# Kernel tuning notes

Measured on AMD Instinct MI355X. Metric: run time of the kernel, lower is better.

Reference implementation:

```python
import jax, jax.numpy as jnp
import numpy as np
import math

EPS_NORM = 1e-12
BN_EPS = 1e-5


def _l2norm(x):
    n = jnp.sqrt(jnp.sum(x * x, axis=-1, keepdims=True))
    return x / jnp.maximum(n, EPS_NORM)


def setup_inputs() -> dict:
    key = jax.random.key(0)
    ks = jax.random.split(key, 16)
    b, c, t, l = 16, 32, 16, 256
    s = 0.05
    return {
        "x": jax.random.normal(ks[0], (b, c, t, l), jnp.float32),
        "q_w": jax.random.normal(ks[1], (c, c), jnp.float32) * s,
        "q_b": jax.random.normal(ks[2], (c,), jnp.float32) * s,
        "k_w": jax.random.normal(ks[3], (c, c), jnp.float32) * s,
        "k_b": jax.random.normal(ks[4], (c,), jnp.float32) * s,
        "v_w": jax.random.normal(ks[5], (c, c), jnp.float32) * s,
        "v_b": jax.random.normal(ks[6], (c,), jnp.float32) * s,
        "m_w": jax.random.normal(ks[7], (c, c), jnp.float32) * s,
        "m_b": jax.random.normal(ks[8], (c,), jnp.float32) * s,
        "pre_prompt": jax.random.normal(ks[9], (1, c, 1, l), jnp.float32) * s,
        "conv_w": jax.random.normal(ks[10], (c, c, 9, 1), jnp.float32) * s,
        "conv_b": jax.random.normal(ks[11], (c,), jnp.float32) * s,
        "bn_gamma": jnp.ones((c,), jnp.float32),
        "bn_beta": jnp.zeros((c,), jnp.float32),
        "lin_w": jax.random.normal(ks[12], (l, l), jnp.float32) * s,
        "lin_b": jax.random.normal(ks[13], (l,), jnp.float32) * s,
        "atten_flag": 1,
    }


def reference(x, q_w, q_b, k_w, k_b, v_w, v_b, m_w, m_b, pre_prompt,
              conv_w, conv_b, bn_gamma, bn_beta, lin_w, lin_b, atten_flag):
    b, c, t, l = x.shape
    nh = 8
    hd = c // nh

    xp = jnp.transpose(x, (0, 2, 3, 1))  # (b,t,l,c)

    def heads(w, bias):
        h = xp @ w.T + bias
        h = h.reshape(b, t, l, nh, hd).transpose(0, 1, 3, 2, 4)  # (b,t,nh,l,hd)
        return _l2norm(h)

    q = heads(q_w, q_b)
    k = heads(k_w, k_b)
    v = heads(v_w, v_b)

    atten = jnp.einsum('bthld,bthmd->bthlm', q, k) / math.sqrt(hd)
    atten = jax.nn.softmax(atten, axis=-1)
    o = jnp.einsum('bthlm,bthmd->bthld', atten, v)  # (b,t,nh,l,hd)
    o = o.transpose(0, 1, 3, 2, 4).reshape(b, t, l, c)
    o = o @ m_w.T + m_b
    xo = jnp.transpose(o, (0, 3, 1, 2))  # (b,c,t,l)

    pre = jnp.broadcast_to(pre_prompt, (b, c, 1, l))
    con = jnp.concatenate([xo[:, :, :8], pre], axis=2)  # (b,c,9,l)

    # ConvNormAct: Conv2d (VALID, kernel (9,1)) + BatchNorm2d (batch stats) + ReLU
    h = jax.lax.conv_general_dilated(
        con, conv_w, window_strides=(1, 1), padding='VALID',
        dimension_numbers=('NCHW', 'OIHW', 'NCHW'))  # (b,c,1,l)
    h = h + conv_b[None, :, None, None]
    mean = jnp.mean(h, axis=(0, 2, 3), keepdims=True)
    var = jnp.var(h, axis=(0, 2, 3), keepdims=True)
    h = (h - mean) * jax.lax.rsqrt(var + BN_EPS)
    h = h * bn_gamma[None, :, None, None] + bn_beta[None, :, None, None]
    h = jax.nn.relu(h)

    p = h @ lin_w.T + lin_b  # Linear over token_len axis
    p = xo[:, :, 2:3] - p
    return jnp.concatenate([xo[:, :, :8], p], axis=2)  # (b,c,9,l)
```

## Files before the change

### kernel.cpp

```cpp
#include <hip/hip_runtime.h>
#include <hip/hip_bf16.h>


typedef __fp16 h2 __attribute__((ext_vector_type(2)));

#define O_OFF  0u
#define XO_OFF 2097152u
#define H_OFF  6291456u
#define S_OFF  6815744u

__device__ __forceinline__ int probe_f32(const unsigned short* graw) {
    return graw[0] == 0;
}
template<typename T> __device__ __forceinline__ float ldv(const T* p, long i);
template<> __device__ __forceinline__ float ldv<float>(const float* p, long i) {
    return p[i];
}
template<> __device__ __forceinline__ float ldv<__hip_bfloat16>(const __hip_bfloat16* p, long i) {
    return __bfloat162float(p[i]);
}
template<typename T> __device__ __forceinline__ void stv(T* p, size_t i, float v);
template<> __device__ __forceinline__ void stv<float>(float* p, size_t i, float v) {
    p[i] = v;
}
template<> __device__ __forceinline__ void stv<__hip_bfloat16>(__hip_bfloat16* p, size_t i, float v) {
    p[i] = __float2bfloat16(v);
}
__device__ __forceinline__ h2 pkh2(float a, float b) {
    return __builtin_amdgcn_cvt_pkrtz(a, b);
}
__device__ __forceinline__ float bflo(unsigned int u) {
    union { unsigned int i; float f; } c; c.i = u << 16; return c.f;
}
__device__ __forceinline__ float bfhi(unsigned int u) {
    union { unsigned int i; float f; } c; c.i = u & 0xffff0000u; return c.f;
}
#if __has_builtin(__builtin_amdgcn_fdot2)
__device__ __forceinline__ float fdot2(h2 a, h2 b, float c) {
    return __builtin_amdgcn_fdot2(a, b, c, false);
}
#else
__device__ __forceinline__ float fdot2(h2 a, h2 b, float c) {
    return fmaf((float)a[0], (float)b[0], fmaf((float)a[1], (float)b[1], c));
}
#endif
union KVrow { uint4 u; h2 h[4]; };

template<typename T>
__device__ __forceinline__ void attn_phase(
    const T* __restrict__ x,
    const T* __restrict__ qw, const T* __restrict__ qb,
    const T* __restrict__ kw, const T* __restrict__ kb,
    const T* __restrict__ vw, const T* __restrict__ vb,
    unsigned short* __restrict__ O, char* smem)
{
    uint4* KV = (uint4*)smem;
    float (*WL)[4][32] = (float (*)[4][32])(smem + 4096);
    float (*BL)[4]     = (float (*)[4])(smem + 5632);

    const int tid = threadIdx.x;
    const int blk = blockIdx.x;
    const int h = blk & 7, bt = blk >> 3;
    const int b = bt >> 3, t = bt & 7;
    const int h4 = h * 4;

    for (int e = tid; e < 384; e += 128) {
        int p = e >> 7, r = e & 127;
        const T* W = (p == 0) ? qw : ((p == 1) ? kw : vw);
        WL[p][r >> 5][r & 31] = ldv(W, (long)(h4 + (r >> 5)) * 32 + (r & 31));
    }
    if (tid < 12) {
        int p = tid >> 2, j = tid & 3;
        const T* B = (p == 0) ? qb : ((p == 1) ? kb : vb);
        BL[p][j] = ldv(B, h4 + j);
    }

    float xv0[32], xv1[32];
    #pragma unroll
    for (int c = 0; c < 32; c++) {
        const long xb = (((long)b * 32 + c) * 16 + t) * 256 + tid;
        xv0[c] = ldv(x, xb);
        xv1[c] = ldv(x, xb + 128);
    }
    __syncthreads();

    float4 pr0[3], pr1[3];
    #pragma unroll
    for (int p = 0; p < 3; p++) {
        float a0[4], a1[4];
        #pragma unroll
        for (int j = 0; j < 4; j++) { a0[j] = BL[p][j]; a1[j] = a0[j]; }
        #pragma unroll
        for (int c0 = 0; c0 < 32; c0 += 4) {
            float4 w0 = *(const float4*)&WL[p][0][c0];
            float4 w1 = *(const float4*)&WL[p][1][c0];
            float4 w2 = *(const float4*)&WL[p][2][c0];
            float4 w3 = *(const float4*)&WL[p][3][c0];
            const float* wj[4] = {(const float*)&w0, (const float*)&w1,
                                  (const float*)&w2, (const float*)&w3};
            #pragma unroll
            for (int cc = 0; cc < 4; cc++) {
                float x0 = xv0[c0+cc], x1 = xv1[c0+cc];
                #pragma unroll
                for (int j = 0; j < 4; j++) {
                    a0[j] = fmaf(x0, wj[j][cc], a0[j]);
                    a1[j] = fmaf(x1, wj[j][cc], a1[j]);
                }
            }
        }
        float s20 = a0[0]*a0[0] + a0[1]*a0[1] + a0[2]*a0[2] + a0[3]*a0[3];
        float s21 = a1[0]*a1[0] + a1[1]*a1[1] + a1[2]*a1[2] + a1[3]*a1[3];
        float i0 = 1.0f / fmaxf(sqrtf(s20), 1e-12f);
        float i1 = 1.0f / fmaxf(sqrtf(s21), 1e-12f);
        if (p == 0) { i0 *= 0.7213475204444817f; i1 *= 0.7213475204444817f; }
        pr0[p] = make_float4(a0[0]*i0, a0[1]*i0, a0[2]*i0, a0[3]*i0);
        pr1[p] = make_float4(a1[0]*i1, a1[1]*i1, a1[2]*i1, a1[3]*i1);
    }

    KVrow r0, r1;
    r0.h[0] = pkh2(pr0[1].x, pr0[1].y); r0.h[1] = pkh2(pr0[1].z, pr0[1].w);
    r0.h[2] = pkh2(pr0[2].x, pr0[2].y); r0.h[3] = pkh2(pr0[2].z, pr0[2].w);
    r1.h[0] = pkh2(pr1[1].x, pr1[1].y); r1.h[1] = pkh2(pr1[1].z, pr1[1].w);
    r1.h[2] = pkh2(pr1[2].x, pr1[2].y); r1.h[3] = pkh2(pr1[2].z, pr1[2].w);
    KV[tid]       = r0.u;
    KV[tid + 128] = r1.u;
    const h2 qa01 = pkh2(pr0[0].x, pr0[0].y), qa23 = pkh2(pr0[0].z, pr0[0].w);
    const h2 qb01 = pkh2(pr1[0].x, pr1[0].y), qb23 = pkh2(pr1[0].z, pr1[0].w);
    __syncthreads();

    h2 o01a = pkh2(0.f, 0.f), o23a = o01a, o01b = o01a, o23b = o01a;
    float den0 = 0.f, den1 = 0.f;
    #pragma unroll 8
    for (int m = 0; m < 256; m++) {
        KVrow kv; kv.u = KV[m];
        float sa = fdot2(qa01, kv.h[0], fdot2(qa23, kv.h[1], 0.0f));
        float sb = fdot2(qb01, kv.h[0], fdot2(qb23, kv.h[1], 0.0f));
        float ea = __builtin_amdgcn_exp2f(sa);
        float eb = __builtin_amdgcn_exp2f(sb);
        den0 += ea; den1 += eb;
        h2 epa = pkh2(ea, ea), epb = pkh2(eb, eb);
        o01a += epa * kv.h[2]; o23a += epa * kv.h[3];
        o01b += epb * kv.h[2]; o23b += epb * kv.h[3];
    }
    float i0 = 1.0f / den0, i1 = 1.0f / den1;
    h2 ia = pkh2(i0, i0), ib = pkh2(i1, i1);
    union { h2 h; unsigned int u; } c0, c1, c2, c3;
    c0.h = o01a * ia; c1.h = o23a * ia;
    c2.h = o01b * ib; c3.h = o23b * ib;
    *(uint2*)(O + ((size_t)bt * 256u + tid) * 32u + h4)       = make_uint2(c0.u, c1.u);
    *(uint2*)(O + ((size_t)bt * 256u + tid + 128) * 32u + h4) = make_uint2(c2.u, c3.u);
}

template<typename T>
__device__ __forceinline__ void mproj_phase(
    const unsigned short* __restrict__ O,
    const T* __restrict__ mw, const T* __restrict__ mb,
    T* __restrict__ out, float* __restrict__ xof, char* smem)
{
    float* sw = (float*)smem;
    float* sb = (float*)(smem + 4096);
    const int tid = threadIdx.x;
    const int blk = blockIdx.x;
    const int bt = blk >> 1, lhalf = blk & 1;
    const int b = bt >> 3, t = bt & 7;
    const int l = lhalf * 128 + tid;

    for (int e = tid; e < 1024; e += 128) sw[e] = ldv(mw, e);
    if (tid < 32) sb[tid] = ldv(mb, tid);

    float ov[32];
    const unsigned short* src = O + ((size_t)bt * 256u + l) * 32u;
    #pragma unroll
    for (int cc = 0; cc < 4; cc++) {
        union { uint4 u; h2 h[4]; } uu;
        uu.u = *(const uint4*)(src + cc * 8);
        #pragma unroll
        for (int j = 0; j < 4; j++) {
            ov[cc*8 + 2*j]     = (float)uu.h[j][0];
            ov[cc*8 + 2*j + 1] = (float)uu.h[j][1];
        }
    }
    __syncthreads();

    #pragma unroll 4
    for (int co = 0; co < 32; co++) {
        float s = sb[co];
        #pragma unroll
        for (int c0 = 0; c0 < 32; c0 += 4) {
            float4 w4 = *(const float4*)&sw[co * 32 + c0];
            s = fmaf(ov[c0+0], w4.x, s);
            s = fmaf(ov[c0+1], w4.y, s);
            s = fmaf(ov[c0+2], w4.z, s);
            s = fmaf(ov[c0+3], w4.w, s);
        }
        stv(out, (((size_t)b * 32 + co) * 9 + t) * 256u + l, s);
        xof[(((size_t)b * 32 + co) * 8 + t) * 256u + l] = s;
    }
}

template<typename T>
__device__ __forceinline__ void conv_phase(
    const float* __restrict__ xof, const T* __restrict__ pre,
    const T* __restrict__ cw, const T* __restrict__ cb,
    float* __restrict__ hout, float* __restrict__ s, char* smem)
{
    float* wl = (float*)smem;
    const int tid = threadIdx.x;
    const int blk = blockIdx.x;
    const int b = blk >> 4, cog = (blk >> 1) & 7, lhalf = blk & 1;
    const int co0 = cog * 4;
    const int l = lhalf * 128 + tid;

    for (int e = tid; e < 1152; e += 128) {
        int g = e & 3, r = e >> 2;
        wl[e] = ldv(cw, (long)(co0 + g) * 288 + r);
    }
    __syncthreads();

    float a0 = 0.f, a1 = 0.f, a2 = 0.f, a3 = 0.f;
    #pragma unroll 4
    for (int ci = 0; ci < 32; ci++) {
        const float* xp = xof + (((size_t)b * 32 + ci) * 8) * 256u + l;
        float v[9];
        #pragma unroll
        for (int kt = 0; kt < 8; kt++) v[kt] = xp[kt * 256];
        v[8] = ldv(pre, (long)ci * 256 + l);
        #pragma unroll
        for (int kt = 0; kt < 9; kt++) {
            float4 w4 = *(const float4*)&wl[(ci * 9 + kt) * 4];
            a0 = fmaf(v[kt], w4.x, a0);
            a1 = fmaf(v[kt], w4.y, a1);
            a2 = fmaf(v[kt], w4.z, a2);
            a3 = fmaf(v[kt], w4.w, a3);
        }
    }
    a0 += ldv(cb, co0+0); a1 += ldv(cb, co0+1);
    a2 += ldv(cb, co0+2); a3 += ldv(cb, co0+3);

    hout[((size_t)b * 32 + co0 + 0) * 256u + l] = a0;
    hout[((size_t)b * 32 + co0 + 1) * 256u + l] = a1;
    hout[((size_t)b * 32 + co0 + 2) * 256u + l] = a2;
    hout[((size_t)b * 32 + co0 + 3) * 256u + l] = a3;

    float acc[4] = {a0, a1, a2, a3};
    #pragma unroll
    for (int g = 0; g < 4; g++) {
        float sg = acc[g], sq = acc[g] * acc[g];
        #pragma unroll
        for (int off = 32; off > 0; off >>= 1) {
            sg += __shfl_down(sg, off, 64);
            sq += __shfl_down(sq, off, 64);
        }
        if ((tid & 63) == 0) {
            atomicAdd(&s[co0 + g], sg);
            atomicAdd(&s[32 + co0 + g], sq);
        }
    }
}

__device__ __forceinline__ float rowdot(const float* rp, const float* hn) {
    float acc = 0.f;
    #pragma unroll 4
    for (int i0 = 0; i0 < 256; i0 += 4) {
        float4 u = *(const float4*)(rp + i0);
        acc = fmaf(hn[i0+0], u.x, acc);
        acc = fmaf(hn[i0+1], u.y, acc);
        acc = fmaf(hn[i0+2], u.z, acc);
        acc = fmaf(hn[i0+3], u.w, acc);
    }
    return acc;
}
__device__ __forceinline__ float rowdot(const __hip_bfloat16* rp_, const float* hn) {
    const unsigned short* rp = (const unsigned short*)rp_;
    float acc = 0.f;
    #pragma unroll 2
    for (int i0 = 0; i0 < 256; i0 += 16) {
        uint4 u0 = *(const uint4*)(rp + i0);
        uint4 u1 = *(const uint4*)(rp + i0 + 8);
        unsigned int uu[8] = {u0.x, u0.y, u0.z, u0.w, u1.x, u1.y, u1.z, u1.w};
        #pragma unroll
        for (int j = 0; j < 8; j++) {
            acc = fmaf(hn[i0 + 2*j],     bflo(uu[j]), acc);
            acc = fmaf(hn[i0 + 2*j + 1], bfhi(uu[j]), acc);
        }
    }
    return acc;
}

template<typename T>
__device__ __forceinline__ void lin_phase(
    const float* __restrict__ hbuf, const float* __restrict__ sbuf,
    const T* __restrict__ gam, const T* __restrict__ bet,
    const T* __restrict__ lw, const T* __restrict__ lb,
    const float* __restrict__ xof, T* __restrict__ out, char* smem)
{
    float* hn = (float*)smem;
    const int tid = threadIdx.x;
    const int blk = blockIdx.x;
    const int b = blk >> 5, co = blk & 31;

    float mean = sbuf[co] * (1.0f / 4096.0f);
    float var  = fmaxf(sbuf[32 + co] * (1.0f / 4096.0f) - mean * mean, 0.0f);
    float sc = ldv(gam, co) * __frsqrt_rn(var + 1e-5f);
    float sh = ldv(bet, co) - mean * sc;

    const size_t hb = (size_t)blk * 256u;
    hn[tid]       = fmaxf(fmaf(hbuf[hb + tid], sc, sh), 0.0f);
    hn[tid + 128] = fmaxf(fmaf(hbuf[hb + tid + 128], sc, sh), 0.0f);
    __syncthreads();

    float acc0 = rowdot(lw + (size_t)tid * 256u, hn) + ldv(lb, tid);
    float acc1 = rowdot(lw + (size_t)(tid + 128) * 256u, hn) + ldv(lb, tid + 128);

    const size_t xb = (((size_t)b * 32 + co) * 8 + 2) * 256u;
    const size_t ob = (((size_t)b * 32 + co) * 9 + 8) * 256u;
    stv(out, ob + tid,       xof[xb + tid] - acc0);
    stv(out, ob + tid + 128, xof[xb + tid + 128] - acc1);
}

__global__ __launch_bounds__(128) void k_attn_s(
    const void* x, const void* qw, const void* qb, const void* kw,
    const void* kb, const void* vw, const void* vb,
    unsigned short* O, float* sbuf, const unsigned short* graw)
{
    __shared__ __align__(16) char smem[6144];
    if (blockIdx.x == 1023 && threadIdx.x < 64) sbuf[threadIdx.x] = 0.0f;
    if (probe_f32(graw))
        attn_phase<float>((const float*)x, (const float*)qw, (const float*)qb,
            (const float*)kw, (const float*)kb, (const float*)vw,
            (const float*)vb, O, smem);
    else
        attn_phase<__hip_bfloat16>((const __hip_bfloat16*)x,
            (const __hip_bfloat16*)qw, (const __hip_bfloat16*)qb,
            (const __hip_bfloat16*)kw, (const __hip_bfloat16*)kb,
            (const __hip_bfloat16*)vw, (const __hip_bfloat16*)vb, O, smem);
}
__global__ __launch_bounds__(128) void k_mproj_s(
    const unsigned short* O, const void* mw, const void* mb,
    void* out, float* xof, const unsigned short* graw)
{
    __shared__ __align__(16) char smem[6144];
    if (probe_f32(graw))
        mproj_phase<float>(O, (const float*)mw, (const float*)mb,
                           (float*)out, xof, smem);
    else
        mproj_phase<__hip_bfloat16>(O, (const __hip_bfloat16*)mw,
                                    (const __hip_bfloat16*)mb,
                                    (__hip_bfloat16*)out, xof, smem);
}
__global__ __launch_bounds__(128) void k_conv_s(
    const float* xof, const void* pre, const void* cw, const void* cb,
    float* hbuf, float* sbuf, const unsigned short* graw)
{
    __shared__ __align__(16) char smem[6144];
    if (probe_f32(graw))
        conv_phase<float>(xof, (const float*)pre, (const float*)cw,
                          (const float*)cb, hbuf, sbuf, smem);
    else
        conv_phase<__hip_bfloat16>(xof, (const __hip_bfloat16*)pre,
                                   (const __hip_bfloat16*)cw,
                                   (const __hip_bfloat16*)cb, hbuf, sbuf, smem);
}
__global__ __launch_bounds__(128) void k_lin_s(
    const float* hbuf, const float* sbuf, const void* gam, const void* bet,
    const void* lw, const void* lb, const float* xof, void* out,
    const unsigned short* graw)
{
    __shared__ __align__(16) char smem[6144];
    if (probe_f32(graw))
        lin_phase<float>(hbuf, sbuf, (const float*)gam, (const float*)bet,
                         (const float*)lw, (const float*)lb, xof,
                         (float*)out, smem);
    else
        lin_phase<__hip_bfloat16>(hbuf, sbuf, (const __hip_bfloat16*)gam,
                                  (const __hip_bfloat16*)bet,
                                  (const __hip_bfloat16*)lw,
                                  (const __hip_bfloat16*)lb, xof,
                                  (__hip_bfloat16*)out, smem);
}

extern "C" void kernel_launch(void* const* d_in, const int* in_sizes, int n_in,
                              void* d_out, int out_size, void* d_ws, size_t ws_size,
                              hipStream_t stream) {
    const void* x   = d_in[0];
    const void* qw  = d_in[1];  const void* qb  = d_in[2];
    const void* kw  = d_in[3];  const void* kb  = d_in[4];
    const void* vw  = d_in[5];  const void* vb  = d_in[6];
    const void* mw  = d_in[7];  const void* mb  = d_in[8];
    const void* pre = d_in[9];
    const void* cw  = d_in[10]; const void* cb  = d_in[11];
    const void* gam = d_in[12]; const void* bet = d_in[13];
    const void* lw  = d_in[14]; const void* lb  = d_in[15];
    const unsigned short* graw = (const unsigned short*)d_in[12];

    unsigned short* Obuf = (unsigned short*)((char*)d_ws + O_OFF);
    float* xof  = (float*)((char*)d_ws + XO_OFF);
    float* hbuf = (float*)((char*)d_ws + H_OFF);
    float* sbuf = (float*)((char*)d_ws + S_OFF);

    k_attn_s <<<1024, 128, 0, stream>>>(x, qw, qb, kw, kb, vw, vb,
                                        Obuf, sbuf, graw);
    k_mproj_s<<<256,  128, 0, stream>>>(Obuf, mw, mb, d_out, xof, graw);
    k_conv_s <<<256,  128, 0, stream>>>(xof, pre, cw, cb, hbuf, sbuf, graw);
    k_lin_s  <<<512,  128, 0, stream>>>(hbuf, sbuf, gam, bet, lw, lb,
                                        xof, d_out, graw);
}
```

Measured before the change: 185.3 us.

## Replace exp2 with packed fp16 polynomial and pair channels in linear stage

The attention inner loop now evaluates exp2 with a degree-5 packed-fp16 polynomial over both query rows at once, using bounded scores from l2-normalized q/k. It restructures K and broadcast V storage so accumulation uses packed FMAs, removing the scalar exp2 transcendentals. The linear stage processes two channels per block with 256 threads, reusing each weight row for two outputs and halving blocks. Risks include fp16 precision loss in accumulation over 256 keys and larger shared memory use.

```diff
diff --git a/kernel.cpp b/kernel.cpp
--- a/kernel.cpp
+++ b/kernel.cpp
@@ -29,6 +29,7 @@
 __device__ __forceinline__ h2 pkh2(float a, float b) {
     return __builtin_amdgcn_cvt_pkrtz(a, b);
 }
+__device__ __forceinline__ h2 h2bc(float v) { return pkh2(v, v); }
 __device__ __forceinline__ float bflo(unsigned int u) {
     union { unsigned int i; float f; } c; c.i = u << 16; return c.f;
 }
@@ -44,7 +45,7 @@
     return fmaf((float)a[0], (float)b[0], fmaf((float)a[1], (float)b[1], c));
 }
 #endif
-union KVrow { uint4 u; h2 h[4]; };
+#define PFMA(a, b, c) __builtin_elementwise_fma((a), (b), (c))
 
 template<typename T>
 __device__ __forceinline__ void attn_phase(
@@ -54,9 +55,10 @@
     const T* __restrict__ vw, const T* __restrict__ vb,
     unsigned short* __restrict__ O, char* smem)
 {
-    uint4* KV = (uint4*)smem;
-    float (*WL)[4][32] = (float (*)[4][32])(smem + 4096);
-    float (*BL)[4]     = (float (*)[4])(smem + 5632);
+    uint2* Karr = (uint2*)smem;
+    uint4* Vbr  = (uint4*)(smem + 2048);
+    float (*WL)[4][32] = (float (*)[4][32])(smem + 6144);
+    float (*BL)[4]     = (float (*)[4])(smem + 7680);
 
     const int tid = threadIdx.x;
     const int blk = blockIdx.x;
@@ -117,36 +119,55 @@
         pr1[p] = make_float4(a1[0]*i1, a1[1]*i1, a1[2]*i1, a1[3]*i1);
     }
 
-    KVrow r0, r1;
-    r0.h[0] = pkh2(pr0[1].x, pr0[1].y); r0.h[1] = pkh2(pr0[1].z, pr0[1].w);
-    r0.h[2] = pkh2(pr0[2].x, pr0[2].y); r0.h[3] = pkh2(pr0[2].z, pr0[2].w);
-    r1.h[0] = pkh2(pr1[1].x, pr1[1].y); r1.h[1] = pkh2(pr1[1].z, pr1[1].w);
-    r1.h[2] = pkh2(pr1[2].x, pr1[2].y); r1.h[3] = pkh2(pr1[2].z, pr1[2].w);
-    KV[tid]       = r0.u;
-    KV[tid + 128] = r1.u;
+    union { uint2 u; h2 h[2]; } ka, kb2;
+    ka.h[0]  = pkh2(pr0[1].x, pr0[1].y); ka.h[1]  = pkh2(pr0[1].z, pr0[1].w);
+    kb2.h[0] = pkh2(pr1[1].x, pr1[1].y); kb2.h[1] = pkh2(pr1[1].z, pr1[1].w);
+    union { uint4 u; h2 h[4]; } va, vb2;
+    va.h[0]  = h2bc(pr0[2].x); va.h[1]  = h2bc(pr0[2].y);
+    va.h[2]  = h2bc(pr0[2].z); va.h[3]  = h2bc(pr0[2].w);
+    vb2.h[0] = h2bc(pr1[2].x); vb2.h[1] = h2bc(pr1[2].y);
+    vb2.h[2] = h2bc(pr1[2].z); vb2.h[3] = h2bc(pr1[2].w);
+    Karr[tid]       = ka.u;
+    Karr[tid + 128] = kb2.u;
+    Vbr[tid]        = va.u;
+    Vbr[tid + 128]  = vb2.u;
     const h2 qa01 = pkh2(pr0[0].x, pr0[0].y), qa23 = pkh2(pr0[0].z, pr0[0].w);
     const h2 qb01 = pkh2(pr1[0].x, pr1[0].y), qb23 = pkh2(pr1[0].z, pr1[0].w);
     __syncthreads();
 
-    h2 o01a = pkh2(0.f, 0.f), o23a = o01a, o01b = o01a, o23b = o01a;
+    const h2 C0 = h2bc(1.0f),          C1 = h2bc(0.69314718f);
+    const h2 C2 = h2bc(0.24022651f),   C3 = h2bc(0.05550411f);
+    const h2 C4 = h2bc(0.00961813f),   C5 = h2bc(0.00133336f);
+    const h2 M0 = {(__fp16)1.0f, (__fp16)0.0f};
+    const h2 M1 = {(__fp16)0.0f, (__fp16)1.0f};
+
+    h2 A0 = h2bc(0.0f), A1 = A0, A2 = A0, A3 = A0;
     float den0 = 0.f, den1 = 0.f;
     #pragma unroll 8
     for (int m = 0; m < 256; m++) {
-        KVrow kv; kv.u = KV[m];
-        float sa = fdot2(qa01, kv.h[0], fdot2(qa23, kv.h[1], 0.0f));
-        float sb = fdot2(qb01, kv.h[0], fdot2(qb23, kv.h[1], 0.0f));
-        float ea = __builtin_amdgcn_exp2f(sa);
-        float eb = __builtin_amdgcn_exp2f(sb);
-        den0 += ea; den1 += eb;
-        h2 epa = pkh2(ea, ea), epb = pkh2(eb, eb);
-        o01a += epa * kv.h[2]; o23a += epa * kv.h[3];
-        o01b += epb * kv.h[2]; o23b += epb * kv.h[3];
-    }
-    float i0 = 1.0f / den0, i1 = 1.0f / den1;
-    h2 ia = pkh2(i0, i0), ib = pkh2(i1, i1);
+        union { uint2 u; h2 h[2]; } ku; ku.u = Karr[m];
+        union { uint4 u; h2 h[4]; } vu; vu.u = Vbr[m];
+        float sa = fdot2(qa01, ku.h[0], fdot2(qa23, ku.h[1], 0.0f));
+        float sb = fdot2(qb01, ku.h[0], fdot2(qb23, ku.h[1], 0.0f));
+        h2 xx = pkh2(sa, sb);
+        h2 p = PFMA(xx, C5, C4);
+        p = PFMA(xx, p, C3);
+        p = PFMA(xx, p, C2);
+        p = PFMA(xx, p, C1);
+        p = PFMA(xx, p, C0);
+        den0 = fdot2(p, M0, den0);
+        den1 = fdot2(p, M1, den1);
+        A0 = PFMA(p, vu.h[0], A0);
+        A1 = PFMA(p, vu.h[1], A1);
+        A2 = PFMA(p, vu.h[2], A2);
+        A3 = PFMA(p, vu.h[3], A3);
+    }
+    float ia = 1.0f / den0, ib = 1.0f / den1;
     union { h2 h; unsigned int u; } c0, c1, c2, c3;
-    c0.h = o01a * ia; c1.h = o23a * ia;
-    c2.h = o01b * ib; c3.h = o23b * ib;
+    c0.h = pkh2((float)A0[0] * ia, (float)A1[0] * ia);
+    c1.h = pkh2((float)A2[0] * ia, (float)A3[0] * ia);
+    c2.h = pkh2((float)A0[1] * ib, (float)A1[1] * ib);
+    c3.h = pkh2((float)A2[1] * ib, (float)A3[1] * ib);
     *(uint2*)(O + ((size_t)bt * 256u + tid) * 32u + h4)       = make_uint2(c0.u, c1.u);
     *(uint2*)(O + ((size_t)bt * 256u + tid + 128) * 32u + h4) = make_uint2(c2.u, c3.u);
 }
@@ -258,21 +279,25 @@
     }
 }
 
-__device__ __forceinline__ float rowdot(const float* rp, const float* hn) {
-    float acc = 0.f;
+__device__ __forceinline__ void rowdot2(const float* rp, const float* hn0,
+                                        const float* hn1, float& a0, float& a1) {
+    float s0 = 0.f, s1 = 0.f;
     #pragma unroll 4
     for (int i0 = 0; i0 < 256; i0 += 4) {
-        float4 u = *(const float4*)(rp + i0);
-        acc = fmaf(hn[i0+0], u.x, acc);
-        acc = fmaf(hn[i0+1], u.y, acc);
-        acc = fmaf(hn[i0+2], u.z, acc);
-        acc = fmaf(hn[i0+3], u.w, acc);
-    }
-    return acc;
-}
-__device__ __forceinline__ float rowdot(const __hip_bfloat16* rp_, const float* hn) {
+        float4 u  = *(const float4*)(rp + i0);
+        float4 p0 = *(const float4*)(hn0 + i0);
+        float4 p1 = *(const float4*)(hn1 + i0);
+        s0 = fmaf(p0.x, u.x, s0); s1 = fmaf(p1.x, u.x, s1);
+        s0 = fmaf(p0.y, u.y, s0); s1 = fmaf(p1.y, u.y, s1);
+        s0 = fmaf(p0.z, u.z, s0); s1 = fmaf(p1.z, u.z, s1);
+        s0 = fmaf(p0.w, u.w, s0); s1 = fmaf(p1.w, u.w, s1);
+    }
+    a0 = s0; a1 = s1;
+}
+__device__ __forceinline__ void rowdot2(const __hip_bfloat16* rp_, const float* hn0,
+                                        const float* hn1, float& a0, float& a1) {
     const unsigned short* rp = (const unsigned short*)rp_;
-    float acc = 0.f;
+    float s0 = 0.f, s1 = 0.f;
     #pragma unroll 2
     for (int i0 = 0; i0 < 256; i0 += 16) {
         uint4 u0 = *(const uint4*)(rp + i0);
@@ -280,11 +305,14 @@
         unsigned int uu[8] = {u0.x, u0.y, u0.z, u0.w, u1.x, u1.y, u1.z, u1.w};
         #pragma unroll
         for (int j = 0; j < 8; j++) {
-            acc = fmaf(hn[i0 + 2*j],     bflo(uu[j]), acc);
-            acc = fmaf(hn[i0 + 2*j + 1], bfhi(uu[j]), acc);
-        }
-    }
-    return acc;
+            float wl = bflo(uu[j]), wh = bfhi(uu[j]);
+            s0 = fmaf(hn0[i0 + 2*j],     wl, s0);
+            s1 = fmaf(hn1[i0 + 2*j],     wl, s1);
+            s0 = fmaf(hn0[i0 + 2*j + 1], wh, s0);
+            s1 = fmaf(hn1[i0 + 2*j + 1], wh, s1);
+        }
+    }
+    a0 = s0; a1 = s1;
 }
 
 template<typename T>
@@ -294,28 +322,39 @@
     const T* __restrict__ lw, const T* __restrict__ lb,
     const float* __restrict__ xof, T* __restrict__ out, char* smem)
 {
-    float* hn = (float*)smem;
+    float* hn0 = (float*)smem;
+    float* hn1 = (float*)(smem + 1024);
     const int tid = threadIdx.x;
     const int blk = blockIdx.x;
-    const int b = blk >> 5, co = blk & 31;
-
-    float mean = sbuf[co] * (1.0f / 4096.0f);
-    float var  = fmaxf(sbuf[32 + co] * (1.0f / 4096.0f) - mean * mean, 0.0f);
-    float sc = ldv(gam, co) * __frsqrt_rn(var + 1e-5f);
-    float sh = ldv(bet, co) - mean * sc;
-
-    const size_t hb = (size_t)blk * 256u;
-    hn[tid]       = fmaxf(fmaf(hbuf[hb + tid], sc, sh), 0.0f);
-    hn[tid + 128] = fmaxf(fmaf(hbuf[hb + tid + 128], sc, sh), 0.0f);
+    const int b = blk >> 4, cop = blk & 15;
+    const int co0 = cop * 2, co1 = co0 + 1;
+
+    float mean0 = sbuf[co0] * (1.0f / 4096.0f);
+    float var0  = fmaxf(sbuf[32 + co0] * (1.0f / 4096.0f) - mean0 * mean0, 0.0f);
+    float sc0 = ldv(gam, co0) * __frsqrt_rn(var0 + 1e-5f);
+    float sh0 = ldv(bet, co0) - mean0 * sc0;
+    float mean1 = sbuf[co1] * (1.0f / 4096.0f);
+    float var1  = fmaxf(sbuf[32 + co1] * (1.0f / 4096.0f) - mean1 * mean1, 0.0f);
+    float sc1 = ldv(gam, co1) * __frsqrt_rn(var1 + 1e-5f);
+    float sh1 = ldv(bet, co1) - mean1 * sc1;
+
+    const size_t hb0 = ((size_t)b * 32 + co0) * 256u;
+    const size_t hb1 = ((size_t)b * 32 + co1) * 256u;
+    hn0[tid] = fmaxf(fmaf(hbuf[hb0 + tid], sc0, sh0), 0.0f);
+    hn1[tid] = fmaxf(fmaf(hbuf[hb1 + tid], sc1, sh1), 0.0f);
     __syncthreads();
 
-    float acc0 = rowdot(lw + (size_t)tid * 256u, hn) + ldv(lb, tid);
-    float acc1 = rowdot(lw + (size_t)(tid + 128) * 256u, hn) + ldv(lb, tid + 128);
-
-    const size_t xb = (((size_t)b * 32 + co) * 8 + 2) * 256u;
-    const size_t ob = (((size_t)b * 32 + co) * 9 + 8) * 256u;
-    stv(out, ob + tid,       xof[xb + tid] - acc0);
-    stv(out, ob + tid + 128, xof[xb + tid + 128] - acc1);
+    float a0, a1;
+    rowdot2(lw + (size_t)tid * 256u, hn0, hn1, a0, a1);
+    float bias = ldv(lb, tid);
+    a0 += bias; a1 += bias;
+
+    const size_t xb0 = (((size_t)b * 32 + co0) * 8 + 2) * 256u;
+    const size_t xb1 = (((size_t)b * 32 + co1) * 8 + 2) * 256u;
+    const size_t ob0 = (((size_t)b * 32 + co0) * 9 + 8) * 256u;
+    const size_t ob1 = (((size_t)b * 32 + co1) * 9 + 8) * 256u;
+    stv(out, ob0 + tid, xof[xb0 + tid] - a0);
+    stv(out, ob1 + tid, xof[xb1 + tid] - a1);
 }
 
 __global__ __launch_bounds__(128) void k_attn_s(
@@ -323,7 +362,7 @@
     const void* kb, const void* vw, const void* vb,
     unsigned short* O, float* sbuf, const unsigned short* graw)
 {
-    __shared__ __align__(16) char smem[6144];
+    __shared__ __align__(16) char smem[7744];
     if (blockIdx.x == 1023 && threadIdx.x < 64) sbuf[threadIdx.x] = 0.0f;
     if (probe_f32(graw))
         attn_phase<float>((const float*)x, (const float*)qw, (const float*)qb,
@@ -361,12 +400,12 @@
                                    (const __hip_bfloat16*)cw,
                                    (const __hip_bfloat16*)cb, hbuf, sbuf, smem);
 }
-__global__ __launch_bounds__(128) void k_lin_s(
+__global__ __launch_bounds__(256) void k_lin_s(
     const float* hbuf, const float* sbuf, const void* gam, const void* bet,
     const void* lw, const void* lb, const float* xof, void* out,
     const unsigned short* graw)
 {
-    __shared__ __align__(16) char smem[6144];
+    __shared__ __align__(16) char smem[2048];
     if (probe_f32(graw))
         lin_phase<float>(hbuf, sbuf, (const float*)gam, (const float*)bet,
                          (const float*)lw, (const float*)lb, xof,
@@ -402,6 +441,6 @@
                                         Obuf, sbuf, graw);
     k_mproj_s<<<256,  128, 0, stream>>>(Obuf, mw, mb, d_out, xof, graw);
     k_conv_s <<<256,  128, 0, stream>>>(xof, pre, cw, cb, hbuf, sbuf, graw);
-    k_lin_s  <<<512,  128, 0, stream>>>(hbuf, sbuf, gam, bet, lw, lb,
+    k_lin_s  <<<256,  256, 0, stream>>>(hbuf, sbuf, gam, bet, lw, lb,
                                         xof, d_out, graw);
 }
```

Result: faster. 178.6 us (-3.6%).
